# Optimization experiments

Measured on AMD Instinct MI355X. Metric: run time of the kernel, lower is better.

Reference implementation:

```python
import jax, jax.numpy as jnp
import numpy as np

N_NODES = 100000
N_EDGES = 1600000
D_H = 64
D_E = 64
D_Q = 64
D_HID = 128
N_GRAPHS = 16


def _mlp_params(key, d_in, d_hid):
    k1, k2, k3, k4 = jax.random.split(key, 4)
    s1 = 1.0 / np.sqrt(d_in)
    s2 = 1.0 / np.sqrt(d_hid)
    return (
        jax.random.uniform(k1, (d_in, d_hid), jnp.float32, -s1, s1),
        jax.random.uniform(k2, (d_hid,), jnp.float32, -s1, s1),
        jax.random.uniform(k3, (d_hid, 1), jnp.float32, -s2, s2),
        jax.random.uniform(k4, (1,), jnp.float32, -s2, s2),
    )


def setup_inputs() -> dict:
    key = jax.random.key(0)
    ks = jax.random.split(key, 8)
    h = jax.random.normal(ks[0], (N_NODES, D_H), jnp.float32)
    e = jax.random.normal(ks[1], (N_EDGES, D_E), jnp.float32)
    q = jax.random.normal(ks[2], (N_GRAPHS, D_Q), jnp.float32)
    edge_index = jax.random.randint(ks[3], (2, N_EDGES), 0, N_NODES, jnp.int64)
    edge_batch = jax.random.randint(ks[4], (N_EDGES,), 0, N_GRAPHS, jnp.int64)
    gw1, gb1, gw2, gb2 = _mlp_params(ks[5], 2 * D_H + D_Q, D_HID)
    sw1, sb1, sw2, sb2 = _mlp_params(ks[6], 2 * D_H + D_E, D_HID)
    return {
        "h": h, "e": e, "q": q,
        "edge_index": edge_index, "edge_batch": edge_batch,
        "gate_w1": gw1, "gate_b1": gb1, "gate_w2": gw2, "gate_b2": gb2,
        "score_w1": sw1, "score_b1": sb1, "score_w2": sw2, "score_b2": sb2,
    }


def _mlp(x, w1, b1, w2, b2):
    # 2-layer MLP, no layernorm (use_layer_norm=False), output dim 1
    hidden = jax.nn.relu(x @ w1 + b1)
    return (hidden @ w2 + b2)[..., 0]


def _dst_softmax(raw, dst, num_nodes):
    # numerically stable per-destination softmax via segment reductions
    max_vals = jax.ops.segment_max(raw, dst, num_segments=num_nodes)
    exp_vals = jnp.exp(raw - max_vals[dst])
    sum_exp = jax.ops.segment_sum(exp_vals, dst, num_segments=num_nodes)
    denom = jnp.maximum(sum_exp[dst], 1e-9)
    return exp_vals / denom


def reference(h, e, q, edge_index, edge_batch,
              gate_w1, gate_b1, gate_w2, gate_b2,
              score_w1, score_b1, score_w2, score_b2):
    src, dst = edge_index[0], edge_index[1]
    h_i = h[src]            # [E, d_h]
    h_j = h[dst]            # [E, d_h]
    q_e = q[edge_batch]     # [E, d_q]
    gate_in = jnp.concatenate([h_i, h_j, q_e], axis=-1)
    gate = jax.nn.sigmoid(_mlp(gate_in, gate_w1, gate_b1, gate_w2, gate_b2))
    score_in = jnp.concatenate([h_i, h_j, e], axis=-1)
    score = _mlp(score_in, score_w1, score_b1, score_w2, score_b2)
    raw = gate * score
    return _dst_softmax(raw, dst, h.shape[0])
```

## Files before the change

kernel.cpp:

```cpp
#include <hip/hip_runtime.h>
#include <hip/hip_bf16.h>

#define NN 100000
#define NE 1600000

typedef __attribute__((ext_vector_type(8))) unsigned short ushort8v;
typedef __attribute__((ext_vector_type(4))) unsigned short ushort4v;
typedef __attribute__((ext_vector_type(8))) short short8v;
typedef __attribute__((ext_vector_type(4))) float f32x4;

__device__ __forceinline__ float b2f(unsigned short u) {
  return __uint_as_float(((unsigned)u) << 16);
}
__device__ __forceinline__ short f2bs(float f) {
  unsigned u = __float_as_uint(f);
  unsigned r = (u + 0x7FFFu + ((u >> 16) & 1u)) >> 16;
  return (short)r;
}

__global__ void qproj_kernel(const float* __restrict__ q,
                             const float* __restrict__ gw1,
                             const float* __restrict__ gb1,
                             float* __restrict__ Qg) {
  int g = blockIdx.x, j = threadIdx.x;
  float acc = gb1[j];
  for (int k = 0; k < 64; ++k) acc += q[g * 64 + k] * gw1[(128 + k) * 128 + j];
  Qg[g * 128 + j] = acc;
}

__global__ __launch_bounds__(1024) void prepack_kernel(
    const float* __restrict__ sw1, short8v* __restrict__ WtG) {
  int tid = threadIdx.x;
  int t = tid >> 7, ks = (tid >> 6) & 1, lane = tid & 63;
  int qg = lane >> 4, cl = lane & 15;
  short8v fr;
#pragma unroll
  for (int j = 0; j < 8; ++j)
    fr[j] = f2bs(sw1[(128 + ks * 32 + qg * 8 + j) * 128 + t * 16 + cl]);
  WtG[tid] = fr;
}

__global__ __launch_bounds__(256) void nodeproj_kernel(
    const float* __restrict__ h, const float* __restrict__ gw1,
    const float* __restrict__ sw1, __hip_bfloat16* __restrict__ GA,
    __hip_bfloat16* __restrict__ GB, __hip_bfloat16* __restrict__ SA,
    __hip_bfloat16* __restrict__ SB) {
  __shared__ float hs[64][64];
  __shared__ float Ws[64][128];
  int part = blockIdx.y;
  const float* W = (part & 1) ? sw1 : gw1;
  int roff = (part >= 2) ? 64 : 0;
  __hip_bfloat16* outp = (part == 0) ? GA : (part == 1) ? SA : (part == 2) ? GB : SB;
  int n0 = blockIdx.x * 64;
  int t = threadIdx.x;

  {
    int n = t & 63, kc = t >> 6;
    int gn = n0 + n;
#pragma unroll
    for (int i = 0; i < 4; ++i) {
      int k = kc * 16 + i * 4;
      float4 hv = make_float4(0.f, 0.f, 0.f, 0.f);
      if (gn < NN) hv = *(const float4*)&h[gn * 64 + k];
      hs[k + 0][n] = hv.x; hs[k + 1][n] = hv.y;
      hs[k + 2][n] = hv.z; hs[k + 3][n] = hv.w;
    }
  }
  {
    const float* Wb = W + roff * 128;
    float* wsf = &Ws[0][0];
#pragma unroll
    for (int i = 0; i < 8; ++i) {
      int flat = (i * 256 + t) * 4;
      *(float4*)&wsf[flat] = *(const float4*)&Wb[flat];
    }
  }
  __syncthreads();

  int tx = t & 31, ty = t >> 5;
  float acc[8][4] = {};
#pragma unroll 4
  for (int k = 0; k < 64; ++k) {
    float hn[8];
    *(float4*)&hn[0] = *(const float4*)&hs[k][ty * 8];
    *(float4*)&hn[4] = *(const float4*)&hs[k][ty * 8 + 4];
    float wv[4];
#pragma unroll
    for (int i = 0; i < 4; ++i) wv[i] = Ws[k][tx + 32 * i];
#pragma unroll
    for (int j = 0; j < 8; ++j)
#pragma unroll
      for (int i = 0; i < 4; ++i) acc[j][i] += hn[j] * wv[i];
  }
#pragma unroll
  for (int j = 0; j < 8; ++j) {
    int gn = n0 + ty * 8 + j;
    if (gn < NN) {
#pragma unroll
      for (int i = 0; i < 4; ++i)
        outp[(size_t)gn * 128 + tx + 32 * i] = __float2bfloat16(acc[j][i]);
    }
  }
}

__global__ __launch_bounds__(256) void gate_kernel(
    const int* __restrict__ eidx, const int* __restrict__ ebat,
    const __hip_bfloat16* __restrict__ GA, const __hip_bfloat16* __restrict__ GB,
    const float* __restrict__ Qg, const float* __restrict__ gw2,
    const float* __restrict__ gb2, float* __restrict__ gate) {
  int ee = blockIdx.x * 256 + threadIdx.x;
  int src = eidx[ee], dst = eidx[NE + ee], g = ebat[ee];
  const ushort8v* ga = (const ushort8v*)((const unsigned short*)GA + (size_t)src * 128);
  const ushort8v* gb = (const ushort8v*)((const unsigned short*)GB + (size_t)dst * 128);
  const f32x4* qv = (const f32x4*)(Qg + g * 128);
  const f32x4* w2 = (const f32x4*)gw2;
  float gacc = 0.f;
#pragma unroll
  for (int h = 0; h < 2; ++h) {
    ushort8v av[8], bv[8];
#pragma unroll
    for (int k = 0; k < 8; ++k) { av[k] = ga[h * 8 + k]; bv[k] = gb[h * 8 + k]; }
#pragma unroll
    for (int k = 0; k < 8; ++k) {
      int jo = h * 8 + k;
#pragma unroll
      for (int half = 0; half < 2; ++half) {
        f32x4 qq = qv[2 * jo + half];
        f32x4 ww = w2[2 * jo + half];
#pragma unroll
        for (int ii = 0; ii < 4; ++ii) {
          float x = b2f(av[k][half * 4 + ii]) + b2f(bv[k][half * 4 + ii]) + qq[ii];
          gacc = fmaf(fmaxf(x, 0.f), ww[ii], gacc);
        }
      }
    }
  }
  gate[ee] = 1.f / (1.f + __expf(-(gacc + gb2[0])));
}

__global__ __launch_bounds__(256) void score_kernel(
    const float* __restrict__ e, const int* __restrict__ eidx,
    const __hip_bfloat16* __restrict__ SA, const __hip_bfloat16* __restrict__ SB,
    const short8v* __restrict__ WtG, const float* __restrict__ sb1,
    const float* __restrict__ sw2, const float* __restrict__ sb2,
    const float* __restrict__ gate, float* __restrict__ out,
    float* __restrict__ nsum) {
  __shared__ short8v WtS[1024];
  __shared__ float sb1S[128], sw2S[128];
  const int tid = threadIdx.x;
  const int w = tid >> 6, lane = tid & 63;
  const int qg = lane >> 4, cl = lane & 15;
  const int EB = blockIdx.x * 256 + w * 64;
  const unsigned short* SAU = (const unsigned short*)SA;
  const unsigned short* SBU = (const unsigned short*)SB;
  const float sb2v = sb2[0];

  {
    const f32x4* s4 = (const f32x4*)WtG;
    f32x4* d4 = (f32x4*)WtS;
#pragma unroll
    for (int i = 0; i < 4; ++i) d4[tid + i * 256] = s4[tid + i * 256];
    if (tid < 128) { sb1S[tid] = sb1[tid]; sw2S[tid] = sw2[tid]; }
  }
  __syncthreads();

#pragma unroll 1
  for (int rt = 0; rt < 4; ++rt) {
    const int erow = EB + rt * 16 + cl;
    const int srcv = eidx[erow];
    const int dstv = eidx[NE + erow];

    const float* ap = e + (size_t)erow * 64 + qg * 8;
    f32x4 f0 = __builtin_nontemporal_load((const f32x4*)(ap + 0));
    f32x4 f1 = __builtin_nontemporal_load((const f32x4*)(ap + 4));
    f32x4 f2 = __builtin_nontemporal_load((const f32x4*)(ap + 32));
    f32x4 f3 = __builtin_nontemporal_load((const f32x4*)(ap + 36));
    short8v b0, b1;
    b0[0] = f2bs(f0.x); b0[1] = f2bs(f0.y); b0[2] = f2bs(f0.z); b0[3] = f2bs(f0.w);
    b0[4] = f2bs(f1.x); b0[5] = f2bs(f1.y); b0[6] = f2bs(f1.z); b0[7] = f2bs(f1.w);
    b1[0] = f2bs(f2.x); b1[1] = f2bs(f2.y); b1[2] = f2bs(f2.z); b1[3] = f2bs(f2.w);
    b1[4] = f2bs(f3.x); b1[5] = f2bs(f3.y); b1[6] = f2bs(f3.z); b1[7] = f2bs(f3.w);

    ushort4v sav[8], sbv[8];
    const unsigned short* sr = SAU + (size_t)srcv * 128 + qg * 4;
    const unsigned short* dr = SBU + (size_t)dstv * 128 + qg * 4;
#pragma unroll
    for (int t = 0; t < 8; ++t) {
      sav[t] = *(const ushort4v*)(sr + t * 16);
      sbv[t] = *(const ushort4v*)(dr + t * 16);
    }

    float part = 0.f;
#pragma unroll
    for (int t = 0; t < 8; ++t) {
      short8v Aw0 = WtS[(t * 2 + 0) * 64 + lane];
      short8v Aw1 = WtS[(t * 2 + 1) * 64 + lane];
      f32x4 acc = (f32x4){0.f, 0.f, 0.f, 0.f};
      acc = __builtin_amdgcn_mfma_f32_16x16x32_bf16(Aw0, b0, acc, 0, 0, 0);
      acc = __builtin_amdgcn_mfma_f32_16x16x32_bf16(Aw1, b1, acc, 0, 0, 0);
      f32x4 b1v = *(const f32x4*)&sb1S[t * 16 + qg * 4];
      f32x4 w2v = *(const f32x4*)&sw2S[t * 16 + qg * 4];
#pragma unroll
      for (int i = 0; i < 4; ++i) {
        float hv = acc[i] + b2f(sav[t][i]) + b2f(sbv[t][i]) + b1v[i];
        part = fmaf(fmaxf(hv, 0.f), w2v[i], part);
      }
    }
    part += __shfl_xor(part, 16, 64);
    part += __shfl_xor(part, 32, 64);
    if (lane < 16) {
      int E = EB + rt * 16 + cl;
      float ex = __expf(gate[E] * (part + sb2v));
      out[E] = ex;
      atomicAdd(&nsum[dstv], ex);
    }
  }
}

__global__ __launch_bounds__(256) void norm_kernel(
    const int* __restrict__ eidx, const float* __restrict__ nodesum,
    float* __restrict__ out) {
  int ee = blockIdx.x * 256 + threadIdx.x;
  int dst = eidx[NE + ee];
  out[ee] = out[ee] / fmaxf(nodesum[dst], 1e-9f);
}

extern "C" void kernel_launch(void* const* d_in, const int* in_sizes, int n_in,
                              void* d_out, int out_size, void* d_ws, size_t ws_size,
                              hipStream_t stream) {
  const float* h   = (const float*)d_in[0];
  const float* e   = (const float*)d_in[1];
  const float* q   = (const float*)d_in[2];
  const int* eidx  = (const int*)d_in[3];
  const int* ebat  = (const int*)d_in[4];
  const float* gw1 = (const float*)d_in[5];
  const float* gb1 = (const float*)d_in[6];
  const float* gw2 = (const float*)d_in[7];
  const float* gb2 = (const float*)d_in[8];
  const float* sw1 = (const float*)d_in[9];
  const float* sb1 = (const float*)d_in[10];
  const float* sw2 = (const float*)d_in[11];
  const float* sb2 = (const float*)d_in[12];
  float* out = (float*)d_out;

  char* ws = (char*)d_ws;
  __hip_bfloat16* GA = (__hip_bfloat16*)ws;
  __hip_bfloat16* GB = (__hip_bfloat16*)(ws + 25600000);
  __hip_bfloat16* SA = (__hip_bfloat16*)(ws + 51200000);
  __hip_bfloat16* SB = (__hip_bfloat16*)(ws + 76800000);
  float* Qg    = (float*)(ws + 102400000);
  short8v* WtG = (short8v*)(ws + 102400000 + 8192);
  float* gateb = (float*)(ws + 102400000 + 8192 + 16384);
  float* nsum  = (float*)(ws + 102400000 + 8192 + 16384 + 6400000);

  (void)hipMemsetAsync(nsum, 0, 400000, stream);
  qproj_kernel<<<dim3(16), dim3(128), 0, stream>>>(q, gw1, gb1, Qg);
  prepack_kernel<<<dim3(1), dim3(1024), 0, stream>>>(sw1, WtG);
  nodeproj_kernel<<<dim3(1563, 4), dim3(256), 0, stream>>>(h, gw1, sw1, GA, GB, SA, SB);
  gate_kernel<<<dim3(NE / 256), dim3(256), 0, stream>>>(eidx, ebat, GA, GB, Qg, gw2, gb2, gateb);
  score_kernel<<<dim3(NE / 256), dim3(256), 0, stream>>>(
      e, eidx, SA, SB, WtG, sb1, sw2, sb2, gateb, out, nsum);
  norm_kernel<<<dim3(NE / 256), dim3(256), 0, stream>>>(eidx, nsum, out);
}
```

Measured before the change: 641.4 us.

## Fuse gate MLP into score edge kernel, dropping gate buffer and separate launch

Merges the per-edge gate computation into the score kernel, so each edge reads its indices once and the gate value is computed in registers instead of being written to and read back from a global buffer. Qg and gate weights are staged in shared memory. This removes one full-edge kernel launch, the index re-reads and the gate array traffic. In exchange the fused kernel issues more gathers per edge and holds more registers, which may lower occupancy.

```diff
diff --git a/kernel.cpp b/kernel.cpp
--- a/kernel.cpp
+++ b/kernel.cpp
@@ -103,64 +103,42 @@
   }
 }
 
-__global__ __launch_bounds__(256) void gate_kernel(
-    const int* __restrict__ eidx, const int* __restrict__ ebat,
+__global__ __launch_bounds__(256) void edge_kernel(
+    const float* __restrict__ e, const int* __restrict__ eidx,
+    const int* __restrict__ ebat,
     const __hip_bfloat16* __restrict__ GA, const __hip_bfloat16* __restrict__ GB,
-    const float* __restrict__ Qg, const float* __restrict__ gw2,
-    const float* __restrict__ gb2, float* __restrict__ gate) {
-  int ee = blockIdx.x * 256 + threadIdx.x;
-  int src = eidx[ee], dst = eidx[NE + ee], g = ebat[ee];
-  const ushort8v* ga = (const ushort8v*)((const unsigned short*)GA + (size_t)src * 128);
-  const ushort8v* gb = (const ushort8v*)((const unsigned short*)GB + (size_t)dst * 128);
-  const f32x4* qv = (const f32x4*)(Qg + g * 128);
-  const f32x4* w2 = (const f32x4*)gw2;
-  float gacc = 0.f;
-#pragma unroll
-  for (int h = 0; h < 2; ++h) {
-    ushort8v av[8], bv[8];
-#pragma unroll
-    for (int k = 0; k < 8; ++k) { av[k] = ga[h * 8 + k]; bv[k] = gb[h * 8 + k]; }
-#pragma unroll
-    for (int k = 0; k < 8; ++k) {
-      int jo = h * 8 + k;
-#pragma unroll
-      for (int half = 0; half < 2; ++half) {
-        f32x4 qq = qv[2 * jo + half];
-        f32x4 ww = w2[2 * jo + half];
-#pragma unroll
-        for (int ii = 0; ii < 4; ++ii) {
-          float x = b2f(av[k][half * 4 + ii]) + b2f(bv[k][half * 4 + ii]) + qq[ii];
-          gacc = fmaf(fmaxf(x, 0.f), ww[ii], gacc);
-        }
-      }
-    }
-  }
-  gate[ee] = 1.f / (1.f + __expf(-(gacc + gb2[0])));
-}
-
-__global__ __launch_bounds__(256) void score_kernel(
-    const float* __restrict__ e, const int* __restrict__ eidx,
     const __hip_bfloat16* __restrict__ SA, const __hip_bfloat16* __restrict__ SB,
-    const short8v* __restrict__ WtG, const float* __restrict__ sb1,
-    const float* __restrict__ sw2, const float* __restrict__ sb2,
-    const float* __restrict__ gate, float* __restrict__ out,
+    const float* __restrict__ Qg, const short8v* __restrict__ WtG,
+    const float* __restrict__ sb1, const float* __restrict__ gw2,
+    const float* __restrict__ gb2, const float* __restrict__ sw2,
+    const float* __restrict__ sb2, float* __restrict__ out,
     float* __restrict__ nsum) {
   __shared__ short8v WtS[1024];
-  __shared__ float sb1S[128], sw2S[128];
+  __shared__ f32x4 QgS[512];
+  __shared__ f32x4 gw2S[32], sb1S[32], sw2S[32];
   const int tid = threadIdx.x;
   const int w = tid >> 6, lane = tid & 63;
   const int qg = lane >> 4, cl = lane & 15;
   const int EB = blockIdx.x * 256 + w * 64;
+  const unsigned short* GAU = (const unsigned short*)GA;
+  const unsigned short* GBU = (const unsigned short*)GB;
   const unsigned short* SAU = (const unsigned short*)SA;
   const unsigned short* SBU = (const unsigned short*)SB;
-  const float sb2v = sb2[0];
+  const float sb2v = sb2[0], gb2v = gb2[0];
 
   {
     const f32x4* s4 = (const f32x4*)WtG;
     f32x4* d4 = (f32x4*)WtS;
 #pragma unroll
     for (int i = 0; i < 4; ++i) d4[tid + i * 256] = s4[tid + i * 256];
-    if (tid < 128) { sb1S[tid] = sb1[tid]; sw2S[tid] = sw2[tid]; }
+    const f32x4* q4 = (const f32x4*)Qg;
+    QgS[tid] = q4[tid];
+    QgS[tid + 256] = q4[tid + 256];
+    if (tid < 32) {
+      gw2S[tid] = ((const f32x4*)gw2)[tid];
+      sb1S[tid] = ((const f32x4*)sb1)[tid];
+      sw2S[tid] = ((const f32x4*)sw2)[tid];
+    }
   }
   __syncthreads();
 
@@ -169,28 +147,34 @@
     const int erow = EB + rt * 16 + cl;
     const int srcv = eidx[erow];
     const int dstv = eidx[NE + erow];
+    const int g = ebat[erow];
 
     const float* ap = e + (size_t)erow * 64 + qg * 8;
     f32x4 f0 = __builtin_nontemporal_load((const f32x4*)(ap + 0));
     f32x4 f1 = __builtin_nontemporal_load((const f32x4*)(ap + 4));
     f32x4 f2 = __builtin_nontemporal_load((const f32x4*)(ap + 32));
     f32x4 f3 = __builtin_nontemporal_load((const f32x4*)(ap + 36));
+
+    const unsigned short* sr = SAU + (size_t)srcv * 128 + qg * 4;
+    const unsigned short* dr = SBU + (size_t)dstv * 128 + qg * 4;
+    const unsigned short* gr = GAU + (size_t)srcv * 128 + qg * 4;
+    const unsigned short* hr = GBU + (size_t)dstv * 128 + qg * 4;
+    ushort4v sav[8], sbv[8], gav[8], gbv[8];
+#pragma unroll
+    for (int t = 0; t < 8; ++t) {
+      sav[t] = *(const ushort4v*)(sr + t * 16);
+      sbv[t] = *(const ushort4v*)(dr + t * 16);
+      gav[t] = *(const ushort4v*)(gr + t * 16);
+      gbv[t] = *(const ushort4v*)(hr + t * 16);
+    }
+
     short8v b0, b1;
     b0[0] = f2bs(f0.x); b0[1] = f2bs(f0.y); b0[2] = f2bs(f0.z); b0[3] = f2bs(f0.w);
     b0[4] = f2bs(f1.x); b0[5] = f2bs(f1.y); b0[6] = f2bs(f1.z); b0[7] = f2bs(f1.w);
     b1[0] = f2bs(f2.x); b1[1] = f2bs(f2.y); b1[2] = f2bs(f2.z); b1[3] = f2bs(f2.w);
     b1[4] = f2bs(f3.x); b1[5] = f2bs(f3.y); b1[6] = f2bs(f3.z); b1[7] = f2bs(f3.w);
 
-    ushort4v sav[8], sbv[8];
-    const unsigned short* sr = SAU + (size_t)srcv * 128 + qg * 4;
-    const unsigned short* dr = SBU + (size_t)dstv * 128 + qg * 4;
-#pragma unroll
-    for (int t = 0; t < 8; ++t) {
-      sav[t] = *(const ushort4v*)(sr + t * 16);
-      sbv[t] = *(const ushort4v*)(dr + t * 16);
-    }
-
-    float part = 0.f;
+    float part = 0.f, gpart = 0.f;
 #pragma unroll
     for (int t = 0; t < 8; ++t) {
       short8v Aw0 = WtS[(t * 2 + 0) * 64 + lane];
@@ -198,19 +182,26 @@
       f32x4 acc = (f32x4){0.f, 0.f, 0.f, 0.f};
       acc = __builtin_amdgcn_mfma_f32_16x16x32_bf16(Aw0, b0, acc, 0, 0, 0);
       acc = __builtin_amdgcn_mfma_f32_16x16x32_bf16(Aw1, b1, acc, 0, 0, 0);
-      f32x4 b1v = *(const f32x4*)&sb1S[t * 16 + qg * 4];
-      f32x4 w2v = *(const f32x4*)&sw2S[t * 16 + qg * 4];
+      f32x4 bb = sb1S[t * 4 + qg];
+      f32x4 ww = sw2S[t * 4 + qg];
+      f32x4 qv = QgS[g * 32 + t * 4 + qg];
+      f32x4 g2 = gw2S[t * 4 + qg];
 #pragma unroll
       for (int i = 0; i < 4; ++i) {
-        float hv = acc[i] + b2f(sav[t][i]) + b2f(sbv[t][i]) + b1v[i];
-        part = fmaf(fmaxf(hv, 0.f), w2v[i], part);
+        float sx = acc[i] + b2f(sav[t][i]) + b2f(sbv[t][i]) + bb[i];
+        part = fmaf(fmaxf(sx, 0.f), ww[i], part);
+        float gx = b2f(gav[t][i]) + b2f(gbv[t][i]) + qv[i];
+        gpart = fmaf(fmaxf(gx, 0.f), g2[i], gpart);
       }
     }
     part += __shfl_xor(part, 16, 64);
     part += __shfl_xor(part, 32, 64);
+    gpart += __shfl_xor(gpart, 16, 64);
+    gpart += __shfl_xor(gpart, 32, 64);
     if (lane < 16) {
       int E = EB + rt * 16 + cl;
-      float ex = __expf(gate[E] * (part + sb2v));
+      float gate = 1.f / (1.f + __expf(-(gpart + gb2v)));
+      float ex = __expf(gate * (part + sb2v));
       out[E] = ex;
       atomicAdd(&nsum[dstv], ex);
     }
@@ -250,15 +241,13 @@
   __hip_bfloat16* SB = (__hip_bfloat16*)(ws + 76800000);
   float* Qg    = (float*)(ws + 102400000);
   short8v* WtG = (short8v*)(ws + 102400000 + 8192);
-  float* gateb = (float*)(ws + 102400000 + 8192 + 16384);
-  float* nsum  = (float*)(ws + 102400000 + 8192 + 16384 + 6400000);
+  float* nsum  = (float*)(ws + 102400000 + 8192 + 16384);
 
   (void)hipMemsetAsync(nsum, 0, 400000, stream);
   qproj_kernel<<<dim3(16), dim3(128), 0, stream>>>(q, gw1, gb1, Qg);
   prepack_kernel<<<dim3(1), dim3(1024), 0, stream>>>(sw1, WtG);
   nodeproj_kernel<<<dim3(1563, 4), dim3(256), 0, stream>>>(h, gw1, sw1, GA, GB, SA, SB);
-  gate_kernel<<<dim3(NE / 256), dim3(256), 0, stream>>>(eidx, ebat, GA, GB, Qg, gw2, gb2, gateb);
-  score_kernel<<<dim3(NE / 256), dim3(256), 0, stream>>>(
-      e, eidx, SA, SB, WtG, sb1, sw2, sb2, gateb, out, nsum);
+  edge_kernel<<<dim3(NE / 256), dim3(256), 0, stream>>>(
+      e, eidx, ebat, GA, GB, SA, SB, Qg, WtG, sb1, gw2, gb2, sw2, sb2, out, nsum);
   norm_kernel<<<dim3(NE / 256), dim3(256), 0, stream>>>(eidx, nsum, out);
 }
```

New measurement: 605.7 us. -5.6%, faster.
